# Kernel tuning notes

Measured on AMD Instinct MI355X. Metric: run time of the kernel, lower is better.

## Reference

```python
import jax, jax.numpy as jnp
import numpy as np

D_MODEL = 256
N_HEADS = 8
N_LEVELS = 4
N_POINTS = 4
DH = D_MODEL // N_HEADS
SHAPES = [(100, 150), (50, 75), (25, 38), (13, 19)]  # per-level (H, W)
BATCH = 2


def setup_inputs() -> dict:
    key = jax.random.key(0)
    ks = jax.random.split(key, 8)
    Lq = sum(h * w for h, w in SHAPES)  # 19947
    d = D_MODEL
    off_dim = N_HEADS * N_LEVELS * N_POINTS * 2
    aw_dim = N_HEADS * N_LEVELS * N_POINTS
    s = 1.0 / np.sqrt(d).astype(np.float32)
    lsi = np.concatenate([[0], np.cumsum([h * w for h, w in SHAPES])[:-1]])
    return {
        "query": jax.random.normal(ks[0], (BATCH, Lq, d), jnp.float32),
        "reference_points": jax.random.uniform(ks[1], (BATCH, Lq, N_LEVELS, 2), jnp.float32),
        "input_flatten": jax.random.normal(ks[2], (BATCH, Lq, d), jnp.float32),
        "input_spatial_shapes": jnp.array(SHAPES, dtype=jnp.int32),
        "input_level_start_index": jnp.array(lsi, dtype=jnp.int32),
        "W_samp": 0.01 * jax.random.normal(ks[3], (off_dim, d), jnp.float32),
        "b_samp": 0.1 * jax.random.normal(ks[4], (off_dim,), jnp.float32),
        "W_attn": s * jax.random.normal(ks[5], (aw_dim, d), jnp.float32),
        "b_attn": jnp.zeros((aw_dim,), jnp.float32),
        "W_val": s * jax.random.normal(ks[6], (d, d), jnp.float32),
        "b_val": jnp.zeros((d,), jnp.float32),
        "W_out": s * jax.random.normal(ks[7], (d, d), jnp.float32),
        "b_out": jnp.zeros((d,), jnp.float32),
    }


def _bilinear(v, grid, Hl, Wl):
    # v: [N, H, Hl*Wl, Dh] flattened level feature map per head
    # grid: [N, H, Q, P, 2] in [-1, 1]; align_corners=False, zero padding
    N, H, Q, P, _ = grid.shape
    Dh = v.shape[-1]
    x = (grid[..., 0] + 1.0) * 0.5 * Wl - 0.5
    y = (grid[..., 1] + 1.0) * 0.5 * Hl - 0.5
    x0 = jnp.floor(x)
    y0 = jnp.floor(y)
    lx = x - x0
    ly = y - y0
    x0i = x0.astype(jnp.int32)
    y0i = y0.astype(jnp.int32)

    def corner(xi, yi, w):
        valid = (xi >= 0) & (xi < Wl) & (yi >= 0) & (yi < Hl)
        idx = jnp.clip(yi, 0, Hl - 1) * Wl + jnp.clip(xi, 0, Wl - 1)
        g = jnp.take_along_axis(v, idx.reshape(N, H, Q * P, 1), axis=2)
        return g.reshape(N, H, Q, P, Dh) * (w * valid)[..., None]

    return (corner(x0i, y0i, (1 - lx) * (1 - ly))
            + corner(x0i + 1, y0i, lx * (1 - ly))
            + corner(x0i, y0i + 1, (1 - lx) * ly)
            + corner(x0i + 1, y0i + 1, lx * ly))


def _forward(query, ref, x, shapes, W_samp, b_samp, W_attn, b_attn, W_val, b_val, W_out, b_out):
    N, Lq, d = query.shape
    H, L, P, Dh = N_HEADS, N_LEVELS, N_POINTS, DH
    # value projection -> [N, H, S, Dh]
    value = (x @ W_val.T + b_val).reshape(N, -1, H, Dh).transpose(0, 2, 1, 3)
    off = (query @ W_samp.T + b_samp).reshape(N, Lq, H, L, P, 2)
    attw = jax.nn.softmax((query @ W_attn.T + b_attn).reshape(N, Lq, H, L * P), axis=-1)
    attw = attw.reshape(N, Lq, H, L, P).transpose(0, 2, 1, 3, 4)  # [N,H,Lq,L,P]
    # offset normalizer is (W, H) per level
    norm = jnp.array([[w, h] for h, w in shapes], dtype=query.dtype)  # [L, 2]
    loc = ref[:, :, None, :, None, :] + off / norm[None, None, None, :, None, :]
    grids = (2.0 * loc - 1.0).transpose(0, 2, 1, 3, 4, 5)  # [N,H,Lq,L,P,2]

    acc = jnp.zeros((N, Lq, H, Dh), query.dtype)
    start = 0
    for lvl, (Hl, Wl) in enumerate(shapes):
        v = value[:, :, start:start + Hl * Wl]  # [N,H,Hl*Wl,Dh]
        start += Hl * Wl
        samp = _bilinear(v, grids[:, :, :, lvl], Hl, Wl)  # [N,H,Lq,P,Dh]
        acc = acc + jnp.einsum('nhqpd,nhqp->nqhd', samp, attw[:, :, :, lvl])
    out = acc.reshape(N, Lq, H * Dh)
    return out @ W_out.T + b_out


def reference(query, reference_points, input_flatten, input_spatial_shapes,
              input_level_start_index, W_samp, b_samp, W_attn, b_attn,
              W_val, b_val, W_out, b_out):
    shapes = [(int(h), int(w)) for h, w in np.asarray(input_spatial_shapes)]
    return _forward(query, reference_points, input_flatten, shapes,
                    W_samp, b_samp, W_attn, b_attn, W_val, b_val, W_out, b_out)
```

## Files before the change

### kernel.cpp

```cpp
#include <hip/hip_runtime.h>
#include <hip/hip_bf16.h>

#define NB 2
#define LQ 19947
#define LV 19947
#define DM 256
#define NH 8
#define NL 4
#define NP 4
#define MROWS (NB*LQ)
#define MPAD  39936
#define QPB 2

__device__ __constant__ int c_lvlH[4] = {100, 50, 25, 13};
__device__ __constant__ int c_lvlW[4] = {150, 75, 38, 19};
__device__ __constant__ int c_lvlS[4] = {0, 15000, 18750, 19700};

typedef __attribute__((ext_vector_type(8))) short short8;
typedef __attribute__((ext_vector_type(4))) float f32x4;
typedef __attribute__((ext_vector_type(2))) float f32x2;

__device__ __forceinline__ unsigned short f2bf(float f) {
  unsigned u = __float_as_uint(f);
  u += 0x7FFFu + ((u >> 16) & 1u);
  return (unsigned short)(u >> 16);
}
__device__ __forceinline__ float bfl(unsigned u) { return __uint_as_float(u << 16); }
__device__ __forceinline__ float bfh(unsigned u) { return __uint_as_float(u & 0xFFFF0000u); }
__device__ __forceinline__ f32x2 up2(unsigned u) {
  f32x2 r; r.x = __uint_as_float(u << 16); r.y = __uint_as_float(u & 0xFFFF0000u); return r;
}
__device__ __forceinline__ unsigned cvtpk(float lo, float hi) {
  unsigned r;
  asm("v_cvt_pk_bf16_f32 %0, %1, %2" : "=v"(r) : "v"(lo), "v"(hi));
  return r;
}

__global__ __launch_bounds__(256) void gemm_front(
    const float* __restrict__ xin, const float* __restrict__ query,
    const float* __restrict__ Wv, const float* __restrict__ Wsamp,
    const float* __restrict__ Wattn,
    const float* __restrict__ b_val, const float* __restrict__ b_samp,
    const float* __restrict__ b_attn,
    unsigned short* __restrict__ value, unsigned short* __restrict__ oc)
{
  const float* Af; const float* Bf; const float* biasp;
  unsigned short* Cp; int Nn, cb, bro;
  if (blockIdx.y < 2) {
    Af = xin; Bf = Wv; cb = blockIdx.y; bro = cb * 128;
    biasp = b_val + cb * 128; Cp = value; Nn = 256;
  } else {
    Af = query; cb = blockIdx.y - 2; Cp = oc; Nn = 384;
    if (cb < 2) { Bf = Wsamp; bro = cb * 128; biasp = b_samp + cb * 128; }
    else        { Bf = Wattn; bro = 0;        biasp = b_attn; }
  }

  __shared__ alignas(16) short As[128 * 32];
  __shared__ alignas(16) short Bs[128 * 32];

  const int t = threadIdx.x;
  const int w = t >> 6, l = t & 63;
  const int wr = w >> 1, wc = w & 1;
  const size_t rowBase = (size_t)blockIdx.x * 128;
  const int colBase = cb * 128;

  const f32x4 z = {0.f, 0.f, 0.f, 0.f};
  f32x4 acc[4][4];
  #pragma unroll
  for (int i = 0; i < 4; ++i)
    #pragma unroll
    for (int j = 0; j < 4; ++j) acc[i][j] = z;

  const int srow = t >> 1;
  const int skh  = (t & 1) * 16;
  const int swzW = (srow & 2) << 2;
  const int arow_ok = ((int)rowBase + srow) < MROWS;
  const float* apBase = Af + ((size_t)rowBase + srow) * 256 + skh;
  const float* bpBase = Bf + (size_t)(bro + srow) * 256 + skh;
  short* pA0 = &As[((srow * 32 + skh) ^ swzW)];
  short* pA1 = &As[((srow * 32 + skh + 8) ^ swzW)];
  short* pB0 = &Bs[((srow * 32 + skh) ^ swzW)];
  short* pB1 = &Bs[((srow * 32 + skh + 8) ^ swzW)];
  const float4 fz4 = make_float4(0.f, 0.f, 0.f, 0.f);

  float4 a0, a1, a2, a3, b0, b1, b2, b3;
#define LOADA(K) do { if (arow_ok) { const float* ap = apBase + (K); \
    a0 = *(const float4*)ap; a1 = *(const float4*)(ap + 4); \
    a2 = *(const float4*)(ap + 8); a3 = *(const float4*)(ap + 12); } \
    else { a0 = fz4; a1 = fz4; a2 = fz4; a3 = fz4; } } while (0)
#define LOADB(K) do { const float* bp = bpBase + (K); \
    b0 = *(const float4*)bp; b1 = *(const float4*)(bp + 4); \
    b2 = *(const float4*)(bp + 8); b3 = *(const float4*)(bp + 12); } while (0)

  LOADA(0); LOADB(0);

  for (int ks = 0; ks < 8; ++ks) {
    __syncthreads();
    uint4 wA0, wA1, wB0, wB1;
    wA0.x = cvtpk(a0.x, a0.y); wA0.y = cvtpk(a0.z, a0.w);
    wA0.z = cvtpk(a1.x, a1.y); wA0.w = cvtpk(a1.z, a1.w);
    wA1.x = cvtpk(a2.x, a2.y); wA1.y = cvtpk(a2.z, a2.w);
    wA1.z = cvtpk(a3.x, a3.y); wA1.w = cvtpk(a3.z, a3.w);
    wB0.x = cvtpk(b0.x, b0.y); wB0.y = cvtpk(b0.z, b0.w);
    wB0.z = cvtpk(b1.x, b1.y); wB0.w = cvtpk(b1.z, b1.w);
    wB1.x = cvtpk(b2.x, b2.y); wB1.y = cvtpk(b2.z, b2.w);
    wB1.z = cvtpk(b3.x, b3.y); wB1.w = cvtpk(b3.z, b3.w);
    *(uint4*)pA0 = wA0; *(uint4*)pA1 = wA1;
    *(uint4*)pB0 = wB0; *(uint4*)pB1 = wB1;
    __syncthreads();
    if (ks < 7) { LOADA((ks + 1) * 32); LOADB((ks + 1) * 32); }
    short8 af[4], bf[4];
    #pragma unroll
    for (int i = 0; i < 4; ++i) {
      af[i] = *(const short8*)&As[(((wr * 64 + i * 16 + (l & 15)) * 32 + (l >> 4) * 8)) ^ ((l & 2) << 2)];
      bf[i] = *(const short8*)&Bs[(((wc * 64 + i * 16 + (l & 15)) * 32 + (l >> 4) * 8)) ^ ((l & 2) << 2)];
    }
    #pragma unroll
    for (int i = 0; i < 4; ++i)
      #pragma unroll
      for (int j = 0; j < 4; ++j)
        acc[i][j] = __builtin_amdgcn_mfma_f32_16x16x32_bf16(bf[j], af[i], acc[i][j], 0, 0, 0);
  }
#undef LOADA
#undef LOADB

  const int row0 = (int)rowBase + wr * 64 + (l & 15);
  const int lc0 = wc * 64 + (l >> 4) * 4;
  const int col0 = colBase + lc0;
  #pragma unroll
  for (int j = 0; j < 4; ++j) {
    const float4 bj = *(const float4*)(biasp + lc0 + j * 16);
    #pragma unroll
    for (int i = 0; i < 4; ++i) {
      const int row = row0 + i * 16;
      uint2 st;
      st.x = (unsigned)f2bf(acc[i][j][0] + bj.x) | ((unsigned)f2bf(acc[i][j][1] + bj.y) << 16);
      st.y = (unsigned)f2bf(acc[i][j][2] + bj.z) | ((unsigned)f2bf(acc[i][j][3] + bj.w) << 16);
      *(uint2*)(Cp + (size_t)row * Nn + col0 + j * 16) = st;
    }
  }
}

__global__ __launch_bounds__(256) void gemm_out(
    const unsigned short* __restrict__ Ab, const float* __restrict__ Wof,
    const float* __restrict__ bias, float* __restrict__ Cp)
{
  __shared__ alignas(16) short As[128 * 32];
  __shared__ alignas(16) short Bs[128 * 32];

  const int t = threadIdx.x;
  const int w = t >> 6, l = t & 63;
  const int wr = w >> 1, wc = w & 1;
  const size_t rowBase = (size_t)blockIdx.x * 128;
  const int colBase = blockIdx.y * 128;

  const f32x4 z = {0.f, 0.f, 0.f, 0.f};
  f32x4 acc[4][4];
  #pragma unroll
  for (int i = 0; i < 4; ++i)
    #pragma unroll
    for (int j = 0; j < 4; ++j) acc[i][j] = z;

  const int lrow = l >> 2;
  const int lcol = (l & 3) * 8;
  const int srow = t >> 1;
  const int skh  = (t & 1) * 16;
  const int swzW = (srow & 2) << 2;
  const float* bpBase = Wof + (size_t)(colBase + srow) * 256 + skh;
  short* pB0 = &Bs[((srow * 32 + skh) ^ swzW)];
  short* pB1 = &Bs[((srow * 32 + skh + 8) ^ swzW)];

  float4 b0, b1, b2, b3;
#define LOADB(K) do { const float* bp = bpBase + (K); \
    b0 = *(const float4*)bp; b1 = *(const float4*)(bp + 4); \
    b2 = *(const float4*)(bp + 8); b3 = *(const float4*)(bp + 12); } while (0)

  LOADB(0);

  for (int ks = 0; ks < 8; ++ks) {
    const int k0 = ks * 32;
    __syncthreads();
    #pragma unroll
    for (int i = 0; i < 2; ++i) {
      const int ii = w * 2 + i;
      const unsigned short* gA = Ab + (rowBase + ii * 16 + lrow) * 256 + k0 + lcol;
      __builtin_amdgcn_global_load_lds(
          (const __attribute__((address_space(1))) void*)gA,
          (__attribute__((address_space(3))) void*)&As[ii * 512], 16, 0, 0);
    }
    uint4 wB0, wB1;
    wB0.x = cvtpk(b0.x, b0.y); wB0.y = cvtpk(b0.z, b0.w);
    wB0.z = cvtpk(b1.x, b1.y); wB0.w = cvtpk(b1.z, b1.w);
    wB1.x = cvtpk(b2.x, b2.y); wB1.y = cvtpk(b2.z, b2.w);
    wB1.z = cvtpk(b3.x, b3.y); wB1.w = cvtpk(b3.z, b3.w);
    *(uint4*)pB0 = wB0; *(uint4*)pB1 = wB1;
    __syncthreads();
    if (ks < 7) LOADB((ks + 1) * 32);
    short8 af[4], bf[4];
    #pragma unroll
    for (int i = 0; i < 4; ++i) {
      af[i] = *(const short8*)&As[(wr * 64 + i * 16 + (l & 15)) * 32 + (l >> 4) * 8];
      bf[i] = *(const short8*)&Bs[(((wc * 64 + i * 16 + (l & 15)) * 32 + (l >> 4) * 8)) ^ ((l & 2) << 2)];
    }
    #pragma unroll
    for (int i = 0; i < 4; ++i)
      #pragma unroll
      for (int j = 0; j < 4; ++j)
        acc[i][j] = __builtin_amdgcn_mfma_f32_16x16x32_bf16(bf[j], af[i], acc[i][j], 0, 0, 0);
  }
#undef LOADB

  const int row0 = (int)rowBase + wr * 64 + (l & 15);
  const int col0 = colBase + wc * 64 + (l >> 4) * 4;
  #pragma unroll
  for (int j = 0; j < 4; ++j) {
    const float4 bj = *(const float4*)(bias + col0 + j * 16);
    #pragma unroll
    for (int i = 0; i < 4; ++i) {
      const int row = row0 + i * 16;
      if (row < MROWS) {
        *(float4*)(Cp + (size_t)row * 256 + col0 + j * 16) =
            make_float4(acc[i][j][0] + bj.x, acc[i][j][1] + bj.y,
                        acc[i][j][2] + bj.z, acc[i][j][3] + bj.w);
      }
    }
  }
}

__global__ __launch_bounds__(128) void msda_sample(
    const unsigned short* __restrict__ value,
    const float* __restrict__ refp,
    const unsigned short* __restrict__ oc,
    unsigned short* __restrict__ accb)
{
  __shared__ float s_aw[QPB][128];
  __shared__ float s_ref[QPB][8];
  __shared__ alignas(16) unsigned s_pk[QPB][NH][17][8];

  const int t = threadIdx.x;
  const int bq0 = blockIdx.x * QPB;

  {
    const int q = t >> 6, i = t & 63;
    const int bq = bq0 + q;
    const unsigned pw = *(const unsigned*)(oc + (size_t)bq * 384 + 256 + i * 2);
    s_aw[q][i * 2 + 0] = bfl(pw);
    s_aw[q][i * 2 + 1] = bfh(pw);
    if (t < QPB * 8) {
      const int q2 = t >> 3, j = t & 7;
      s_ref[q2][j] = refp[(size_t)(bq0 + q2) * 8 + j];
    }
  }
  __syncthreads();

  if (t < QPB * NH) {
    const int q = t >> 3, h = t & 7;
    float* aw = &s_aw[q][h * 16];
    float m = aw[0];
    #pragma unroll
    for (int i = 1; i < 16; ++i) m = fmaxf(m, aw[i]);
    float e[16]; float s = 0.f;
    #pragma unroll
    for (int i = 0; i < 16; ++i) { e[i] = __expf(aw[i] - m); s += e[i]; }
    const float inv = 1.f / s;
    #pragma unroll
    for (int i = 0; i < 16; ++i) aw[i] = e[i] * inv;
  }
  __syncthreads();

  #pragma unroll
  for (int it = t; it < QPB * 128; it += 128) {
    const int q = it >> 7, rem = it & 127;
    const int h = rem >> 4, idx = rem & 15;
    const int l = idx >> 2;
    const int bq = bq0 + q;
    const unsigned po = *(const unsigned*)(oc + (size_t)bq * 384 + rem * 2);
    const int Hl = c_lvlH[l], Wl = c_lvlW[l], st = c_lvlS[l];
    const float x = s_ref[q][l * 2 + 0] * (float)Wl - 0.5f + bfl(po);
    const float y = s_ref[q][l * 2 + 1] * (float)Hl - 0.5f + bfh(po);
    const float aw = s_aw[q][rem];
    const float x0f = floorf(x), y0f = floorf(y);
    const float lx = x - x0f, ly = y - y0f;
    const int x0 = (int)x0f, y0 = (int)y0f;
    const float vx0 = (x0 >= 0 && x0 < Wl) ? 1.f : 0.f;
    const float vx1 = (x0 >= -1 && x0 < Wl - 1) ? 1.f : 0.f;
    const float vy0 = (y0 >= 0 && y0 < Hl) ? 1.f : 0.f;
    const float vy1 = (y0 >= -1 && y0 < Hl - 1) ? 1.f : 0.f;
    const int xc0 = min(max(x0, 0), Wl - 1);
    const int xc1 = min(max(x0 + 1, 0), Wl - 1);
    const int yc0 = min(max(y0, 0), Hl - 1);
    const int yc1 = min(max(y0 + 1, 0), Hl - 1);
    const int r0 = st + yc0 * Wl, r1 = st + yc1 * Wl;
    uint4 g0, g1;
    g0.x = (unsigned)(r0 + xc0) * 512u;
    g0.y = (unsigned)(r0 + xc1) * 512u;
    g0.z = __float_as_uint((1.f - lx) * (1.f - ly) * aw * (vx0 * vy0));
    g0.w = __float_as_uint(lx * (1.f - ly) * aw * (vx1 * vy0));
    g1.x = (unsigned)(r1 + xc0) * 512u;
    g1.y = (unsigned)(r1 + xc1) * 512u;
    g1.z = __float_as_uint((1.f - lx) * ly * aw * (vx0 * vy1));
    g1.w = __float_as_uint(lx * ly * aw * (vx1 * vy1));
    *(uint4*)&s_pk[q][h][idx][0] = g0;
    *(uint4*)&s_pk[q][h][idx][4] = g1;
  }
  __syncthreads();

  const int wv = t >> 6;
  const int lane = t & 63;
  const int bq = bq0 + wv;
  const int n = bq / LQ;
  const char* vbase = (const char*)value + (size_t)n * LV * 512;
  const int h = lane >> 3;
  const int c2 = (lane >> 2) & 1;
  const unsigned laneoff = (unsigned)(h * 64 + (lane & 3) * 16);

  f32x2 acc0 = {0.f, 0.f}, acc1 = {0.f, 0.f}, acc2 = {0.f, 0.f}, acc3 = {0.f, 0.f};

#define PKRD(i) (*(const uint4*)&s_pk[wv][h][(i)][c2 * 4])
#define GLD(o)  (*(const uint4*)(vbase + (o) + laneoff))

  uint4 pk0 = PKRD(0), pk1 = PKRD(1), pk2 = PKRD(2), pk3 = PKRD(3);
  uint4 va0 = GLD(pk0.x), vb0 = GLD(pk0.y);
  uint4 va1 = GLD(pk1.x), vb1 = GLD(pk1.y);
  uint4 va2 = GLD(pk2.x), vb2 = GLD(pk2.y);

  #pragma unroll
  for (int idx = 0; idx < 16; ++idx) {
    uint4 va3, vb3, pk4;
    if (idx < 13) { va3 = GLD(pk3.x); vb3 = GLD(pk3.y); }
    if (idx < 12) { pk4 = PKRD(idx + 4); }
    const float was = __uint_as_float(pk0.z);
    const float wbs = __uint_as_float(pk0.w);
    f32x2 wa; wa.x = was; wa.y = was;
    f32x2 wb; wb.x = wbs; wb.y = wbs;
    acc0 = acc0 + wa * up2(va0.x);
    acc1 = acc1 + wa * up2(va0.y);
    acc2 = acc2 + wa * up2(va0.z);
    acc3 = acc3 + wa * up2(va0.w);
    acc0 = acc0 + wb * up2(vb0.x);
    acc1 = acc1 + wb * up2(vb0.y);
    acc2 = acc2 + wb * up2(vb0.z);
    acc3 = acc3 + wb * up2(vb0.w);
    pk0 = pk1; pk1 = pk2; pk2 = pk3; pk3 = pk4;
    va0 = va1; va1 = va2; va2 = va3;
    vb0 = vb1; vb1 = vb2; vb2 = vb3;
  }
#undef PKRD
#undef GLD

  acc0.x += __shfl_xor(acc0.x, 4); acc0.y += __shfl_xor(acc0.y, 4);
  acc1.x += __shfl_xor(acc1.x, 4); acc1.y += __shfl_xor(acc1.y, 4);
  acc2.x += __shfl_xor(acc2.x, 4); acc2.y += __shfl_xor(acc2.y, 4);
  acc3.x += __shfl_xor(acc3.x, 4); acc3.y += __shfl_xor(acc3.y, 4);

  if (c2 == 0) {
    uint4 st;
    st.x = (unsigned)f2bf(acc0.x) | ((unsigned)f2bf(acc0.y) << 16);
    st.y = (unsigned)f2bf(acc1.x) | ((unsigned)f2bf(acc1.y) << 16);
    st.z = (unsigned)f2bf(acc2.x) | ((unsigned)f2bf(acc2.y) << 16);
    st.w = (unsigned)f2bf(acc3.x) | ((unsigned)f2bf(acc3.y) << 16);
    *(uint4*)((char*)accb + (size_t)bq * 512 + laneoff) = st;
  }
}

extern "C" void kernel_launch(void* const* d_in, const int* in_sizes, int n_in,
                              void* d_out, int out_size, void* d_ws, size_t ws_size,
                              hipStream_t stream) {
  const float* query  = (const float*)d_in[0];
  const float* refp   = (const float*)d_in[1];
  const float* xin    = (const float*)d_in[2];
  const float* W_samp = (const float*)d_in[5];
  const float* b_samp = (const float*)d_in[6];
  const float* W_attn = (const float*)d_in[7];
  const float* b_attn = (const float*)d_in[8];
  const float* W_val  = (const float*)d_in[9];
  const float* b_val  = (const float*)d_in[10];
  const float* W_out  = (const float*)d_in[11];
  const float* b_out  = (const float*)d_in[12];
  float* out = (float*)d_out;
  (void)in_sizes; (void)n_in; (void)out_size; (void)ws_size;

  char* ws = (char*)d_ws;
  unsigned short* value = (unsigned short*)(ws);
  unsigned short* accb  = (unsigned short*)(ws + 20447232);
  unsigned short* oc    = (unsigned short*)(ws + 40894464);

  hipLaunchKernelGGL(gemm_front, dim3(312, 5), dim3(256), 0, stream,
                     xin, query, W_val, W_samp, W_attn, b_val, b_samp, b_attn,
                     value, oc);
  hipLaunchKernelGGL(msda_sample, dim3(MROWS / QPB), dim3(128), 0, stream,
                     value, refp, oc, accb);
  hipLaunchKernelGGL(gemm_out, dim3(312, 2), dim3(256), 0, stream,
                     accb, W_out, b_out, out);
}
```

Before: 247.1 us.

## Double-buffer LDS tiles in both GEMMs with one barrier per k-step

```diff
diff --git a/kernel.cpp b/kernel.cpp
--- a/kernel.cpp
+++ b/kernel.cpp
@@ -55,8 +55,8 @@
     else        { Bf = Wattn; bro = 0;        biasp = b_attn; }
   }
 
-  __shared__ alignas(16) short As[128 * 32];
-  __shared__ alignas(16) short Bs[128 * 32];
+  __shared__ alignas(16) short As[2][128 * 32];
+  __shared__ alignas(16) short Bs[2][128 * 32];
 
   const int t = threadIdx.x;
   const int w = t >> 6, l = t & 63;
@@ -73,14 +73,12 @@
 
   const int srow = t >> 1;
   const int skh  = (t & 1) * 16;
-  const int swzW = (srow & 2) << 2;
+  const int swz  = (srow & 6) << 2;
+  const int sc0  = skh ^ swz;
+  const int sc1  = (skh + 8) ^ swz;
   const int arow_ok = ((int)rowBase + srow) < MROWS;
   const float* apBase = Af + ((size_t)rowBase + srow) * 256 + skh;
   const float* bpBase = Bf + (size_t)(bro + srow) * 256 + skh;
-  short* pA0 = &As[((srow * 32 + skh) ^ swzW)];
-  short* pA1 = &As[((srow * 32 + skh + 8) ^ swzW)];
-  short* pB0 = &Bs[((srow * 32 + skh) ^ swzW)];
-  short* pB1 = &Bs[((srow * 32 + skh + 8) ^ swzW)];
   const float4 fz4 = make_float4(0.f, 0.f, 0.f, 0.f);
 
   float4 a0, a1, a2, a3, b0, b1, b2, b3;
@@ -91,38 +89,49 @@
 #define LOADB(K) do { const float* bp = bpBase + (K); \
     b0 = *(const float4*)bp; b1 = *(const float4*)(bp + 4); \
     b2 = *(const float4*)(bp + 8); b3 = *(const float4*)(bp + 12); } while (0)
+#define STAGE(BUF) do { \
+    uint4 wA0, wA1, wB0, wB1; \
+    wA0.x = cvtpk(a0.x, a0.y); wA0.y = cvtpk(a0.z, a0.w); \
+    wA0.z = cvtpk(a1.x, a1.y); wA0.w = cvtpk(a1.z, a1.w); \
+    wA1.x = cvtpk(a2.x, a2.y); wA1.y = cvtpk(a2.z, a2.w); \
+    wA1.z = cvtpk(a3.x, a3.y); wA1.w = cvtpk(a3.z, a3.w); \
+    wB0.x = cvtpk(b0.x, b0.y); wB0.y = cvtpk(b0.z, b0.w); \
+    wB0.z = cvtpk(b1.x, b1.y); wB0.w = cvtpk(b1.z, b1.w); \
+    wB1.x = cvtpk(b2.x, b2.y); wB1.y = cvtpk(b2.z, b2.w); \
+    wB1.z = cvtpk(b3.x, b3.y); wB1.w = cvtpk(b3.z, b3.w); \
+    *(uint4*)&As[BUF][srow * 32 + sc0] = wA0; \
+    *(uint4*)&As[BUF][srow * 32 + sc1] = wA1; \
+    *(uint4*)&Bs[BUF][srow * 32 + sc0] = wB0; \
+    *(uint4*)&Bs[BUF][srow * 32 + sc1] = wB1; } while (0)
 
   LOADA(0); LOADB(0);
+  STAGE(0);
+  LOADA(32); LOADB(32);
+  __syncthreads();
 
   for (int ks = 0; ks < 8; ++ks) {
-    __syncthreads();
-    uint4 wA0, wA1, wB0, wB1;
-    wA0.x = cvtpk(a0.x, a0.y); wA0.y = cvtpk(a0.z, a0.w);
-    wA0.z = cvtpk(a1.x, a1.y); wA0.w = cvtpk(a1.z, a1.w);
-    wA1.x = cvtpk(a2.x, a2.y); wA1.y = cvtpk(a2.z, a2.w);
-    wA1.z = cvtpk(a3.x, a3.y); wA1.w = cvtpk(a3.z, a3.w);
-    wB0.x = cvtpk(b0.x, b0.y); wB0.y = cvtpk(b0.z, b0.w);
-    wB0.z = cvtpk(b1.x, b1.y); wB0.w = cvtpk(b1.z, b1.w);
-    wB1.x = cvtpk(b2.x, b2.y); wB1.y = cvtpk(b2.z, b2.w);
-    wB1.z = cvtpk(b3.x, b3.y); wB1.w = cvtpk(b3.z, b3.w);
-    *(uint4*)pA0 = wA0; *(uint4*)pA1 = wA1;
-    *(uint4*)pB0 = wB0; *(uint4*)pB1 = wB1;
-    __syncthreads();
-    if (ks < 7) { LOADA((ks + 1) * 32); LOADB((ks + 1) * 32); }
+    const int cur = ks & 1;
+    if (ks < 7) STAGE(cur ^ 1);
+    if (ks < 6) { LOADA((ks + 2) * 32); LOADB((ks + 2) * 32); }
     short8 af[4], bf[4];
     #pragma unroll
     for (int i = 0; i < 4; ++i) {
-      af[i] = *(const short8*)&As[(((wr * 64 + i * 16 + (l & 15)) * 32 + (l >> 4) * 8)) ^ ((l & 2) << 2)];
-      bf[i] = *(const short8*)&Bs[(((wc * 64 + i * 16 + (l & 15)) * 32 + (l >> 4) * 8)) ^ ((l & 2) << 2)];
+      const int ar = wr * 64 + i * 16 + (l & 15);
+      const int br = wc * 64 + i * 16 + (l & 15);
+      const int cs = (l >> 4) * 8;
+      af[i] = *(const short8*)&As[cur][ar * 32 + (cs ^ ((ar & 6) << 2))];
+      bf[i] = *(const short8*)&Bs[cur][br * 32 + (cs ^ ((br & 6) << 2))];
     }
     #pragma unroll
     for (int i = 0; i < 4; ++i)
       #pragma unroll
       for (int j = 0; j < 4; ++j)
         acc[i][j] = __builtin_amdgcn_mfma_f32_16x16x32_bf16(bf[j], af[i], acc[i][j], 0, 0, 0);
+    __syncthreads();
   }
 #undef LOADA
 #undef LOADB
+#undef STAGE
 
   const int row0 = (int)rowBase + wr * 64 + (l & 15);
   const int lc0 = wc * 64 + (l >> 4) * 4;
@@ -145,8 +154,8 @@
     const unsigned short* __restrict__ Ab, const float* __restrict__ Wof,
     const float* __restrict__ bias, float* __restrict__ Cp)
 {
-  __shared__ alignas(16) short As[128 * 32];
-  __shared__ alignas(16) short Bs[128 * 32];
+  __shared__ alignas(16) short As[2][128 * 32];
+  __shared__ alignas(16) short Bs[2][128 * 32];
 
   const int t = threadIdx.x;
   const int w = t >> 6, l = t & 63;
@@ -161,54 +170,60 @@
     #pragma unroll
     for (int j = 0; j < 4; ++j) acc[i][j] = z;
 
-  const int lrow = l >> 2;
-  const int lcol = (l & 3) * 8;
   const int srow = t >> 1;
   const int skh  = (t & 1) * 16;
-  const int swzW = (srow & 2) << 2;
+  const int swz  = (srow & 6) << 2;
+  const int sc0  = skh ^ swz;
+  const int sc1  = (skh + 8) ^ swz;
+  const unsigned short* apBase = Ab + ((size_t)rowBase + srow) * 256 + skh;
   const float* bpBase = Wof + (size_t)(colBase + srow) * 256 + skh;
-  short* pB0 = &Bs[((srow * 32 + skh) ^ swzW)];
-  short* pB1 = &Bs[((srow * 32 + skh + 8) ^ swzW)];
-
+
+  uint4 av0, av1;
   float4 b0, b1, b2, b3;
+#define LOADA(K) do { const unsigned short* ap = apBase + (K); \
+    av0 = *(const uint4*)ap; av1 = *(const uint4*)(ap + 8); } while (0)
 #define LOADB(K) do { const float* bp = bpBase + (K); \
     b0 = *(const float4*)bp; b1 = *(const float4*)(bp + 4); \
     b2 = *(const float4*)(bp + 8); b3 = *(const float4*)(bp + 12); } while (0)
-
-  LOADB(0);
+#define STAGE(BUF) do { \
+    uint4 wB0, wB1; \
+    wB0.x = cvtpk(b0.x, b0.y); wB0.y = cvtpk(b0.z, b0.w); \
+    wB0.z = cvtpk(b1.x, b1.y); wB0.w = cvtpk(b1.z, b1.w); \
+    wB1.x = cvtpk(b2.x, b2.y); wB1.y = cvtpk(b2.z, b2.w); \
+    wB1.z = cvtpk(b3.x, b3.y); wB1.w = cvtpk(b3.z, b3.w); \
+    *(uint4*)&As[BUF][srow * 32 + sc0] = av0; \
+    *(uint4*)&As[BUF][srow * 32 + sc1] = av1; \
+    *(uint4*)&Bs[BUF][srow * 32 + sc0] = wB0; \
+    *(uint4*)&Bs[BUF][srow * 32 + sc1] = wB1; } while (0)
+
+  LOADA(0); LOADB(0);
+  STAGE(0);
+  LOADA(32); LOADB(32);
+  __syncthreads();
 
   for (int ks = 0; ks < 8; ++ks) {
-    const int k0 = ks * 32;
-    __syncthreads();
-    #pragma unroll
-    for (int i = 0; i < 2; ++i) {
-      const int ii = w * 2 + i;
-      const unsigned short* gA = Ab + (rowBase + ii * 16 + lrow) * 256 + k0 + lcol;
-      __builtin_amdgcn_global_load_lds(
-          (const __attribute__((address_space(1))) void*)gA,
-          (__attribute__((address_space(3))) void*)&As[ii * 512], 16, 0, 0);
-    }
-    uint4 wB0, wB1;
-    wB0.x = cvtpk(b0.x, b0.y); wB0.y = cvtpk(b0.z, b0.w);
-    wB0.z = cvtpk(b1.x, b1.y); wB0.w = cvtpk(b1.z, b1.w);
-    wB1.x = cvtpk(b2.x, b2.y); wB1.y = cvtpk(b2.z, b2.w);
-    wB1.z = cvtpk(b3.x, b3.y); wB1.w = cvtpk(b3.z, b3.w);
-    *(uint4*)pB0 = wB0; *(uint4*)pB1 = wB1;
-    __syncthreads();
-    if (ks < 7) LOADB((ks + 1) * 32);
+    const int cur = ks & 1;
+    if (ks < 7) STAGE(cur ^ 1);
+    if (ks < 6) { LOADA((ks + 2) * 32); LOADB((ks + 2) * 32); }
     short8 af[4], bf[4];
     #pragma unroll
     for (int i = 0; i < 4; ++i) {
-      af[i] = *(const short8*)&As[(wr * 64 + i * 16 + (l & 15)) * 32 + (l >> 4) * 8];
-      bf[i] = *(const short8*)&Bs[(((wc * 64 + i * 16 + (l & 15)) * 32 + (l >> 4) * 8)) ^ ((l & 2) << 2)];
+      const int ar = wr * 64 + i * 16 + (l & 15);
+      const int br = wc * 64 + i * 16 + (l & 15);
+      const int cs = (l >> 4) * 8;
+      af[i] = *(const short8*)&As[cur][ar * 32 + (cs ^ ((ar & 6) << 2))];
+      bf[i] = *(const short8*)&Bs[cur][br * 32 + (cs ^ ((br & 6) << 2))];
     }
     #pragma unroll
     for (int i = 0; i < 4; ++i)
       #pragma unroll
       for (int j = 0; j < 4; ++j)
         acc[i][j] = __builtin_amdgcn_mfma_f32_16x16x32_bf16(bf[j], af[i], acc[i][j], 0, 0, 0);
-  }
+    __syncthreads();
+  }
+#undef LOADA
 #undef LOADB
+#undef STAGE
 
   const int row0 = (int)rowBase + wr * 64 + (l & 15);
   const int col0 = colBase + wc * 64 + (l >> 4) * 4;
```

Result: no change. 250.9 us (+1.5%).

## Stage full weight tile in LDS once and stream A fragments from registers

Applied to the files above, without the earlier changes.

```diff
diff --git a/kernel.cpp b/kernel.cpp
--- a/kernel.cpp
+++ b/kernel.cpp
@@ -35,8 +35,14 @@
   asm("v_cvt_pk_bf16_f32 %0, %1, %2" : "=v"(r) : "v"(lo), "v"(hi));
   return r;
 }
-
-__global__ __launch_bounds__(256) void gemm_front(
+__device__ __forceinline__ short8 cvt8(const float4& x, const float4& y) {
+  union { uint4 u; short8 s; } v;
+  v.u.x = cvtpk(x.x, x.y); v.u.y = cvtpk(x.z, x.w);
+  v.u.z = cvtpk(y.x, y.y); v.u.w = cvtpk(y.z, y.w);
+  return v.s;
+}
+
+__global__ __launch_bounds__(256, 2) void gemm_front(
     const float* __restrict__ xin, const float* __restrict__ query,
     const float* __restrict__ Wv, const float* __restrict__ Wsamp,
     const float* __restrict__ Wattn,
@@ -54,174 +60,200 @@
     if (cb < 2) { Bf = Wsamp; bro = cb * 128; biasp = b_samp + cb * 128; }
     else        { Bf = Wattn; bro = 0;        biasp = b_attn; }
   }
-
-  __shared__ alignas(16) short As[128 * 32];
-  __shared__ alignas(16) short Bs[128 * 32];
+  const int colBase = cb * 128;
+
+  __shared__ alignas(16) short Bs[128 * 256];
 
   const int t = threadIdx.x;
-  const int w = t >> 6, l = t & 63;
-  const int wr = w >> 1, wc = w & 1;
   const size_t rowBase = (size_t)blockIdx.x * 128;
-  const int colBase = cb * 128;
-
+
+  const int wv = t >> 6, l = t & 63;
+  const int row0 = (int)rowBase + wv * 32 + (l & 15);
+  const int r0c = row0 < MROWS - 1 ? row0 : MROWS - 1;
+  const int r1c = row0 + 16 < MROWS - 1 ? row0 + 16 : MROWS - 1;
+  const int kq = (l >> 4) * 8;
+  const float* a0p = Af + (size_t)r0c * 256 + kq;
+  const float* a1p = Af + (size_t)r1c * 256 + kq;
+
+  float4 c00, c01, c10, c11, n00, n01, n10, n11;
+#define LDA(s00,s01,s10,s11,KS) do { \
+    const float* p0 = a0p + (KS) * 32; const float* p1 = a1p + (KS) * 32; \
+    s00 = *(const float4*)p0; s01 = *(const float4*)(p0 + 4); \
+    s10 = *(const float4*)p1; s11 = *(const float4*)(p1 + 4); } while (0)
+  LDA(c00, c01, c10, c11, 0);
+  LDA(n00, n01, n10, n11, 1);
+
+  {
+    const int c   = t >> 1;
+    const int kh2 = (t & 1) * 32;
+    const int swz = (c & 3) << 4;
+    const float* wp = Bf + (size_t)(bro + c) * 256 + (t & 1) * 16;
+    char* cbp = (char*)Bs + c * 512;
+    float4 q0, q1, q2, q3, r0, r1, r2, r3;
+#define LDW(d0,d1,d2,d3,S) do { const float* p = wp + (S) * 32; \
+    d0 = *(const float4*)p;       d1 = *(const float4*)(p + 4); \
+    d2 = *(const float4*)(p + 8); d3 = *(const float4*)(p + 12); } while (0)
+#define STW(d0,d1,d2,d3,S) do { uint4 w0, w1; \
+    w0.x = cvtpk(d0.x, d0.y); w0.y = cvtpk(d0.z, d0.w); \
+    w0.z = cvtpk(d1.x, d1.y); w0.w = cvtpk(d1.z, d1.w); \
+    w1.x = cvtpk(d2.x, d2.y); w1.y = cvtpk(d2.z, d2.w); \
+    w1.z = cvtpk(d3.x, d3.y); w1.w = cvtpk(d3.z, d3.w); \
+    *(uint4*)(cbp + (S) * 64 + ((kh2 +  0) ^ swz)) = w0; \
+    *(uint4*)(cbp + (S) * 64 + ((kh2 + 16) ^ swz)) = w1; } while (0)
+    LDW(q0, q1, q2, q3, 0); LDW(r0, r1, r2, r3, 1);
+    #pragma unroll
+    for (int s = 0; s < 8; s += 2) {
+      STW(q0, q1, q2, q3, s);     if (s + 2 < 8) LDW(q0, q1, q2, q3, s + 2);
+      STW(r0, r1, r2, r3, s + 1); if (s + 3 < 8) LDW(r0, r1, r2, r3, s + 3);
+    }
+#undef LDW
+#undef STW
+  }
+  __syncthreads();
+
+  const char* lb = (const char*)Bs + (l & 15) * 512 + (((l >> 4) * 16) ^ ((l & 3) << 4));
+
+  f32x4 acc[2][8];
   const f32x4 z = {0.f, 0.f, 0.f, 0.f};
-  f32x4 acc[4][4];
-  #pragma unroll
-  for (int i = 0; i < 4; ++i)
-    #pragma unroll
-    for (int j = 0; j < 4; ++j) acc[i][j] = z;
-
-  const int srow = t >> 1;
-  const int skh  = (t & 1) * 16;
-  const int swzW = (srow & 2) << 2;
-  const int arow_ok = ((int)rowBase + srow) < MROWS;
-  const float* apBase = Af + ((size_t)rowBase + srow) * 256 + skh;
-  const float* bpBase = Bf + (size_t)(bro + srow) * 256 + skh;
-  short* pA0 = &As[((srow * 32 + skh) ^ swzW)];
-  short* pA1 = &As[((srow * 32 + skh + 8) ^ swzW)];
-  short* pB0 = &Bs[((srow * 32 + skh) ^ swzW)];
-  short* pB1 = &Bs[((srow * 32 + skh + 8) ^ swzW)];
-  const float4 fz4 = make_float4(0.f, 0.f, 0.f, 0.f);
-
-  float4 a0, a1, a2, a3, b0, b1, b2, b3;
-#define LOADA(K) do { if (arow_ok) { const float* ap = apBase + (K); \
-    a0 = *(const float4*)ap; a1 = *(const float4*)(ap + 4); \
-    a2 = *(const float4*)(ap + 8); a3 = *(const float4*)(ap + 12); } \
-    else { a0 = fz4; a1 = fz4; a2 = fz4; a3 = fz4; } } while (0)
-#define LOADB(K) do { const float* bp = bpBase + (K); \
-    b0 = *(const float4*)bp; b1 = *(const float4*)(bp + 4); \
-    b2 = *(const float4*)(bp + 8); b3 = *(const float4*)(bp + 12); } while (0)
-
-  LOADA(0); LOADB(0);
-
+  #pragma unroll
+  for (int fi = 0; fi < 2; ++fi)
+    #pragma unroll
+    for (int j = 0; j < 8; ++j) acc[fi][j] = z;
+
+  short8 bq[8], bn[8];
+  #pragma unroll
+  for (int j = 0; j < 8; ++j) bq[j] = *(const short8*)(lb + j * 8192);
+
+  #pragma unroll
   for (int ks = 0; ks < 8; ++ks) {
-    __syncthreads();
-    uint4 wA0, wA1, wB0, wB1;
-    wA0.x = cvtpk(a0.x, a0.y); wA0.y = cvtpk(a0.z, a0.w);
-    wA0.z = cvtpk(a1.x, a1.y); wA0.w = cvtpk(a1.z, a1.w);
-    wA1.x = cvtpk(a2.x, a2.y); wA1.y = cvtpk(a2.z, a2.w);
-    wA1.z = cvtpk(a3.x, a3.y); wA1.w = cvtpk(a3.z, a3.w);
-    wB0.x = cvtpk(b0.x, b0.y); wB0.y = cvtpk(b0.z, b0.w);
-    wB0.z = cvtpk(b1.x, b1.y); wB0.w = cvtpk(b1.z, b1.w);
-    wB1.x = cvtpk(b2.x, b2.y); wB1.y = cvtpk(b2.z, b2.w);
-    wB1.z = cvtpk(b3.x, b3.y); wB1.w = cvtpk(b3.z, b3.w);
-    *(uint4*)pA0 = wA0; *(uint4*)pA1 = wA1;
-    *(uint4*)pB0 = wB0; *(uint4*)pB1 = wB1;
-    __syncthreads();
-    if (ks < 7) { LOADA((ks + 1) * 32); LOADB((ks + 1) * 32); }
-    short8 af[4], bf[4];
-    #pragma unroll
-    for (int i = 0; i < 4; ++i) {
-      af[i] = *(const short8*)&As[(((wr * 64 + i * 16 + (l & 15)) * 32 + (l >> 4) * 8)) ^ ((l & 2) << 2)];
-      bf[i] = *(const short8*)&Bs[(((wc * 64 + i * 16 + (l & 15)) * 32 + (l >> 4) * 8)) ^ ((l & 2) << 2)];
-    }
-    #pragma unroll
-    for (int i = 0; i < 4; ++i)
+    if (ks < 7) {
       #pragma unroll
-      for (int j = 0; j < 4; ++j)
-        acc[i][j] = __builtin_amdgcn_mfma_f32_16x16x32_bf16(bf[j], af[i], acc[i][j], 0, 0, 0);
-  }
-#undef LOADA
-#undef LOADB
-
-  const int row0 = (int)rowBase + wr * 64 + (l & 15);
-  const int lc0 = wc * 64 + (l >> 4) * 4;
-  const int col0 = colBase + lc0;
-  #pragma unroll
-  for (int j = 0; j < 4; ++j) {
-    const float4 bj = *(const float4*)(biasp + lc0 + j * 16);
-    #pragma unroll
-    for (int i = 0; i < 4; ++i) {
-      const int row = row0 + i * 16;
+      for (int j = 0; j < 8; ++j) bn[j] = *(const short8*)(lb + j * 8192 + (ks + 1) * 64);
+    }
+    const short8 af0 = cvt8(c00, c01);
+    const short8 af1 = cvt8(c10, c11);
+    c00 = n00; c01 = n01; c10 = n10; c11 = n11;
+    if (ks < 6) LDA(n00, n01, n10, n11, ks + 2);
+    #pragma unroll
+    for (int j = 0; j < 8; ++j) {
+      acc[0][j] = __builtin_amdgcn_mfma_f32_16x16x32_bf16(bq[j], af0, acc[0][j], 0, 0, 0);
+      acc[1][j] = __builtin_amdgcn_mfma_f32_16x16x32_bf16(bq[j], af1, acc[1][j], 0, 0, 0);
+    }
+    #pragma unroll
+    for (int j = 0; j < 8; ++j) bq[j] = bn[j];
+  }
+#undef LDA
+
+  const int lc = (l >> 4) * 4;
+  #pragma unroll
+  for (int j = 0; j < 8; ++j) {
+    const float4 bj = *(const float4*)(biasp + j * 16 + lc);
+    #pragma unroll
+    for (int fi = 0; fi < 2; ++fi) {
+      const int row = row0 + fi * 16;
       uint2 st;
-      st.x = (unsigned)f2bf(acc[i][j][0] + bj.x) | ((unsigned)f2bf(acc[i][j][1] + bj.y) << 16);
-      st.y = (unsigned)f2bf(acc[i][j][2] + bj.z) | ((unsigned)f2bf(acc[i][j][3] + bj.w) << 16);
-      *(uint2*)(Cp + (size_t)row * Nn + col0 + j * 16) = st;
-    }
-  }
-}
-
-__global__ __launch_bounds__(256) void gemm_out(
+      st.x = (unsigned)f2bf(acc[fi][j][0] + bj.x) | ((unsigned)f2bf(acc[fi][j][1] + bj.y) << 16);
+      st.y = (unsigned)f2bf(acc[fi][j][2] + bj.z) | ((unsigned)f2bf(acc[fi][j][3] + bj.w) << 16);
+      *(uint2*)(Cp + (size_t)row * Nn + colBase + j * 16 + lc) = st;
+    }
+  }
+}
+
+__global__ __launch_bounds__(256, 2) void gemm_out(
     const unsigned short* __restrict__ Ab, const float* __restrict__ Wof,
     const float* __restrict__ bias, float* __restrict__ Cp)
 {
-  __shared__ alignas(16) short As[128 * 32];
-  __shared__ alignas(16) short Bs[128 * 32];
+  __shared__ alignas(16) short Bs[128 * 256];
 
   const int t = threadIdx.x;
-  const int w = t >> 6, l = t & 63;
-  const int wr = w >> 1, wc = w & 1;
   const size_t rowBase = (size_t)blockIdx.x * 128;
   const int colBase = blockIdx.y * 128;
 
+  const int wv = t >> 6, l = t & 63;
+  const int row0 = (int)rowBase + wv * 32 + (l & 15);
+  const int kq = (l >> 4) * 8;
+  const unsigned short* a0p = Ab + (size_t)row0 * 256 + kq;
+  const unsigned short* a1p = a0p + 16 * 256;
+
+  short8 afc0, afc1, afn0, afn1;
+#define LDA2(d0,d1,KS) do { \
+    d0 = *(const short8*)(a0p + (KS) * 32); \
+    d1 = *(const short8*)(a1p + (KS) * 32); } while (0)
+  LDA2(afc0, afc1, 0);
+  LDA2(afn0, afn1, 1);
+
+  {
+    const int c   = t >> 1;
+    const int kh2 = (t & 1) * 32;
+    const int swz = (c & 3) << 4;
+    const float* wp = Wof + (size_t)(colBase + c) * 256 + (t & 1) * 16;
+    char* cbp = (char*)Bs + c * 512;
+    float4 q0, q1, q2, q3, r0, r1, r2, r3;
+#define LDW(d0,d1,d2,d3,S) do { const float* p = wp + (S) * 32; \
+    d0 = *(const float4*)p;       d1 = *(const float4*)(p + 4); \
+    d2 = *(const float4*)(p + 8); d3 = *(const float4*)(p + 12); } while (0)
+#define STW(d0,d1,d2,d3,S) do { uint4 w0, w1; \
+    w0.x = cvtpk(d0.x, d0.y); w0.y = cvtpk(d0.z, d0.w); \
+    w0.z = cvtpk(d1.x, d1.y); w0.w = cvtpk(d1.z, d1.w); \
+    w1.x = cvtpk(d2.x, d2.y); w1.y = cvtpk(d2.z, d2.w); \
+    w1.z = cvtpk(d3.x, d3.y); w1.w = cvtpk(d3.z, d3.w); \
+    *(uint4*)(cbp + (S) * 64 + ((kh2 +  0) ^ swz)) = w0; \
+    *(uint4*)(cbp + (S) * 64 + ((kh2 + 16) ^ swz)) = w1; } while (0)
+    LDW(q0, q1, q2, q3, 0); LDW(r0, r1, r2, r3, 1);
+    #pragma unroll
+    for (int s = 0; s < 8; s += 2) {
+      STW(q0, q1, q2, q3, s);     if (s + 2 < 8) LDW(q0, q1, q2, q3, s + 2);
+      STW(r0, r1, r2, r3, s + 1); if (s + 3 < 8) LDW(r0, r1, r2, r3, s + 3);
+    }
+#undef LDW
+#undef STW
+  }
+  __syncthreads();
+
+  const char* lb = (const char*)Bs + (l & 15) * 512 + (((l >> 4) * 16) ^ ((l & 3) << 4));
+
+  f32x4 acc[2][8];
   const f32x4 z = {0.f, 0.f, 0.f, 0.f};
-  f32x4 acc[4][4];
-  #pragma unroll
-  for (int i = 0; i < 4; ++i)
-    #pragma unroll
-    for (int j = 0; j < 4; ++j) acc[i][j] = z;
-
-  const int lrow = l >> 2;
-  const int lcol = (l & 3) * 8;
-  const int srow = t >> 1;
-  const int skh  = (t & 1) * 16;
-  const int swzW = (srow & 2) << 2;
-  const float* bpBase = Wof + (size_t)(colBase + srow) * 256 + skh;
-  short* pB0 = &Bs[((srow * 32 + skh) ^ swzW)];
-  short* pB1 = &Bs[((srow * 32 + skh + 8) ^ swzW)];
-
-  float4 b0, b1, b2, b3;
-#define LOADB(K) do { const float* bp = bpBase + (K); \
-    b0 = *(const float4*)bp; b1 = *(const float4*)(bp + 4); \
-    b2 = *(const float4*)(bp + 8); b3 = *(const float4*)(bp + 12); } while (0)
-
-  LOADB(0);
-
+  #pragma unroll
+  for (int fi = 0; fi < 2; ++fi)
+    #pragma unroll
+    for (int j = 0; j < 8; ++j) acc[fi][j] = z;
+
+  short8 bq[8], bn[8];
+  #pragma unroll
+  for (int j = 0; j < 8; ++j) bq[j] = *(const short8*)(lb + j * 8192);
+
+  #pragma unroll
   for (int ks = 0; ks < 8; ++ks) {
-    const int k0 = ks * 32;
-    __syncthreads();
-    #pragma unroll
-    for (int i = 0; i < 2; ++i) {
-      const int ii = w * 2 + i;
-      const unsigned short* gA = Ab + (rowBase + ii * 16 + lrow) * 256 + k0 + lcol;
-      __builtin_amdgcn_global_load_lds(
-          (const __attribute__((address_space(1))) void*)gA,
-          (__attribute__((address_space(3))) void*)&As[ii * 512], 16, 0, 0);
-    }
-    uint4 wB0, wB1;
-    wB0.x = cvtpk(b0.x, b0.y); wB0.y = cvtpk(b0.z, b0.w);
-    wB0.z = cvtpk(b1.x, b1.y); wB0.w = cvtpk(b1.z, b1.w);
-    wB1.x = cvtpk(b2.x, b2.y); wB1.y = cvtpk(b2.z, b2.w);
-    wB1.z = cvtpk(b3.x, b3.y); wB1.w = cvtpk(b3.z, b3.w);
-    *(uint4*)pB0 = wB0; *(uint4*)pB1 = wB1;
-    __syncthreads();
-    if (ks < 7) LOADB((ks + 1) * 32);
-    short8 af[4], bf[4];
-    #pragma unroll
-    for (int i = 0; i < 4; ++i) {
-      af[i] = *(const short8*)&As[(wr * 64 + i * 16 + (l & 15)) * 32 + (l >> 4) * 8];
-      bf[i] = *(const short8*)&Bs[(((wc * 64 + i * 16 + (l & 15)) * 32 + (l >> 4) * 8)) ^ ((l & 2) << 2)];
-    }
-    #pragma unroll
-    for (int i = 0; i < 4; ++i)
+    if (ks < 7) {
       #pragma unroll
-      for (int j = 0; j < 4; ++j)
-        acc[i][j] = __builtin_amdgcn_mfma_f32_16x16x32_bf16(bf[j], af[i], acc[i][j], 0, 0, 0);
-  }
-#undef LOADB
-
-  const int row0 = (int)rowBase + wr * 64 + (l & 15);
-  const int col0 = colBase + wc * 64 + (l >> 4) * 4;
-  #pragma unroll
-  for (int j = 0; j < 4; ++j) {
-    const float4 bj = *(const float4*)(bias + col0 + j * 16);
-    #pragma unroll
-    for (int i = 0; i < 4; ++i) {
-      const int row = row0 + i * 16;
+      for (int j = 0; j < 8; ++j) bn[j] = *(const short8*)(lb + j * 8192 + (ks + 1) * 64);
+    }
+    const short8 af0 = afc0;
+    const short8 af1 = afc1;
+    afc0 = afn0; afc1 = afn1;
+    if (ks < 6) LDA2(afn0, afn1, ks + 2);
+    #pragma unroll
+    for (int j = 0; j < 8; ++j) {
+      acc[0][j] = __builtin_amdgcn_mfma_f32_16x16x32_bf16(bq[j], af0, acc[0][j], 0, 0, 0);
+      acc[1][j] = __builtin_amdgcn_mfma_f32_16x16x32_bf16(bq[j], af1, acc[1][j], 0, 0, 0);
+    }
+    #pragma unroll
+    for (int j = 0; j < 8; ++j) bq[j] = bn[j];
+  }
+#undef LDA2
+
+  const int lc = (l >> 4) * 4;
+  #pragma unroll
+  for (int j = 0; j < 8; ++j) {
+    const float4 bj = *(const float4*)(bias + colBase + j * 16 + lc);
+    #pragma unroll
+    for (int fi = 0; fi < 2; ++fi) {
+      const int row = row0 + fi * 16;
       if (row < MROWS) {
-        *(float4*)(Cp + (size_t)row * 256 + col0 + j * 16) =
-            make_float4(acc[i][j][0] + bj.x, acc[i][j][1] + bj.y,
-                        acc[i][j][2] + bj.z, acc[i][j][3] + bj.w);
+        *(float4*)(Cp + (size_t)row * 256 + colBase + j * 16 + lc) =
+            make_float4(acc[fi][j][0] + bj.x, acc[fi][j][1] + bj.y,
+                        acc[fi][j][2] + bj.z, acc[fi][j][3] + bj.w);
       }
     }
   }
```

Measured after the change: 256.4 us. 3.7% more time.
